# Kernel optimization log

Measured on AMD Instinct MI355X. Metric: run time of the kernel, lower is better.

Reference implementation:

```python
import jax, jax.numpy as jnp
import numpy as np

B, P, E, D = 256, 2048, 16, 2
HID, OUT = 128, 128
BN_EPS = 1e-5


def setup_inputs() -> dict:
    key = jax.random.key(0)
    ks = jax.random.split(key, 16)
    inp = {
        "barcode_h0": jax.random.normal(ks[0], (B, P, D), jnp.float32),
        "barcode_h0_count": jax.random.randint(ks[1], (B,), 0, P),
        "barcode_h1": jax.random.normal(ks[2], (B, P, D), jnp.float32),
        "barcode_h1_count": jax.random.randint(ks[3], (B,), 0, P),
        # SLayer params (one per homology dim): centers ~ U[0,1), log_sharpness = log(3.0)
        "centers0": jax.random.uniform(ks[4], (E, D), jnp.float32),
        "log_sharp0": jnp.full((E, D), np.log(3.0), jnp.float32),
        "centers1": jax.random.uniform(ks[5], (E, D), jnp.float32),
        "log_sharp1": jnp.full((E, D), np.log(3.0), jnp.float32),
        # head: Linear(2E -> HID, no bias), BN, ReLU, Linear(HID -> OUT, no bias), BN
        "W1": jax.random.normal(ks[6], (2 * E, HID), jnp.float32) / np.sqrt(2 * E),
        "gamma1": jnp.ones((HID,), jnp.float32),
        "beta1": jnp.zeros((HID,), jnp.float32),
        "W2": jax.random.normal(ks[7], (HID, OUT), jnp.float32) / np.sqrt(HID),
        "gamma2": jnp.ones((OUT,), jnp.float32),
        "beta2": jnp.zeros((OUT,), jnp.float32),
    }
    return inp


def _slayer(pts, counts, centers, log_sharp):
    # pts: [B,P,2], counts: [B], centers/log_sharp: [E,2]
    sharp = jax.nn.softplus(log_sharp) + 1e-6                       # [E,2]
    diff = pts[:, :, None, :] - centers[None, None, :, :]           # [B,P,E,2]
    resp = jnp.exp(-jnp.sum(sharp * diff * diff, axis=-1))          # [B,P,E]
    mask = (jnp.arange(pts.shape[1])[None, :] < counts[:, None]).astype(resp.dtype)
    return jnp.sum(resp * mask[:, :, None], axis=1)                 # [B,E]


def _batchnorm_train(x, gamma, beta):
    m = jnp.mean(x, axis=0)
    v = jnp.var(x, axis=0)  # biased, as torch uses for normalization
    return (x - m) * jax.lax.rsqrt(v + BN_EPS) * gamma + beta


def reference(barcode_h0, barcode_h0_count, barcode_h1, barcode_h1_count,
              centers0, log_sharp0, centers1, log_sharp1,
              W1, gamma1, beta1, W2, gamma2, beta2):
    f0 = _slayer(barcode_h0, barcode_h0_count, centers0, log_sharp0)  # [B,E]
    f1 = _slayer(barcode_h1, barcode_h1_count, centers1, log_sharp1)  # [B,E]
    x = jnp.concatenate([f0, f1], axis=1)                             # [B,2E]
    h = jax.nn.relu(_batchnorm_train(x @ W1, gamma1, beta1))          # [B,HID]
    y = _batchnorm_train(h @ W2, gamma2, beta2)                       # [B,OUT]
    norm = jnp.maximum(jnp.linalg.norm(y, axis=1, keepdims=True), 1e-12)
    return y / norm
```

## Files before the change

### kernel.cpp

```cpp
#include <hip/hip_runtime.h>

#define Bsz 256
#define Pn  2048
#define En  16
#define HIDn 128
#define OUTn 128
#define BN_EPS 1e-5f
#define NREP 16
#define POISON_I ((int)0xAAAAAAAA)


__device__ __forceinline__ void bar_sync(int* ctr) {
    __syncthreads();
    if (threadIdx.x == 0) {
        atomicCAS(ctr, POISON_I, 0);
        __hip_atomic_fetch_add(ctr, 1, __ATOMIC_RELEASE, __HIP_MEMORY_SCOPE_AGENT);
        while (__hip_atomic_load(ctr, __ATOMIC_RELAXED, __HIP_MEMORY_SCOPE_AGENT) < Bsz) {
            __builtin_amdgcn_s_sleep(1);
        }
    }
    __syncthreads();
}

__device__ __forceinline__ float coh_load(const float* p) {
    return __hip_atomic_load(p, __ATOMIC_RELAXED, __HIP_MEMORY_SCOPE_AGENT);
}

__global__ __launch_bounds__(256) void k_fused(
    const float* __restrict__ pts0, const int* __restrict__ cnt0,
    const float* __restrict__ pts1, const int* __restrict__ cnt1,
    const float* __restrict__ c0, const float* __restrict__ ls0,
    const float* __restrict__ c1, const float* __restrict__ ls1,
    const float* __restrict__ W1,
    const float* __restrict__ g1, const float* __restrict__ be1,
    const float* __restrict__ W2,
    const float* __restrict__ g2, const float* __restrict__ be2,
    float* __restrict__ stats,
    int* __restrict__ bars,
    float* __restrict__ out)
{
    __shared__ float4 cs[2][En];
    __shared__ float red[4][32];
    __shared__ float xrow[32];
    __shared__ float hrow[HIDn];
    __shared__ float part[4];

    const int tid = threadIdx.x;
    const int b   = blockIdx.x;

    float* sum1R   = stats;
    float* sumsq1R = stats + NREP * HIDn;
    float* sum2R   = stats + 2 * NREP * HIDn;
    float* sumsq2R = stats + 3 * NREP * HIDn;
    const int rep = (b & (NREP - 1)) * HIDn;

    if (tid < 32) {
        int h = tid >> 4, e = tid & 15;
        const float* C = h ? c1 : c0;
        const float* L = h ? ls1 : ls0;
        float zx = L[2 * e], zy = L[2 * e + 1];
        float sx = (zx > 20.f) ? zx : logf(1.f + expf(zx));
        float sy = (zy > 20.f) ? zy : logf(1.f + expf(zy));
        cs[h][e] = make_float4(C[2 * e], C[2 * e + 1], sx + 1e-6f, sy + 1e-6f);
    }
    __syncthreads();

    const int n0 = cnt0[b];
    const int n1 = cnt1[b];
    const float4* q0 = (const float4*)(pts0 + (size_t)b * Pn * 2);
    const float4* q1 = (const float4*)(pts1 + (size_t)b * Pn * 2);

    float4 f0[4], f1[4];
    #pragma unroll
    for (int i = 0; i < 4; i++) {
        f0[i] = q0[tid + (i << 8)];
        f1[i] = q1[tid + (i << 8)];
    }

    float g1v = 0.f, b1v = 0.f, g2v = 0.f, b2v = 0.f;
    if (tid < HIDn) { g1v = g1[tid]; b1v = be1[tid]; g2v = g2[tid]; b2v = be2[tid]; }

    float m0a[4], m0b[4], m1a[4], m1b[4];
    #pragma unroll
    for (int i = 0; i < 4; i++) {
        int p = (tid + (i << 8)) << 1;
        m0a[i] = (p     < n0) ? 1.f : 0.f;
        m0b[i] = (p + 1 < n0) ? 1.f : 0.f;
        m1a[i] = (p     < n1) ? 1.f : 0.f;
        m1b[i] = (p + 1 < n1) ? 1.f : 0.f;
    }

    float acc0[En], acc1[En];
    #pragma unroll
    for (int e = 0; e < En; e++) { acc0[e] = 0.f; acc1[e] = 0.f; }

    #pragma unroll
    for (int e = 0; e < En; e++) {
        float4 c = cs[0][e];
        float4 d = cs[1][e];
        float a0 = acc0[e], a1 = acc1[e];
        #pragma unroll
        for (int i = 0; i < 4; i++) {
            float dx, dy;
            dx = f0[i].x - c.x; dy = f0[i].y - c.y;
            a0 = fmaf(m0a[i], __expf(-(c.z * dx * dx + c.w * dy * dy)), a0);
            dx = f0[i].z - c.x; dy = f0[i].w - c.y;
            a0 = fmaf(m0b[i], __expf(-(c.z * dx * dx + c.w * dy * dy)), a0);
            dx = f1[i].x - d.x; dy = f1[i].y - d.y;
            a1 = fmaf(m1a[i], __expf(-(d.z * dx * dx + d.w * dy * dy)), a1);
            dx = f1[i].z - d.x; dy = f1[i].w - d.y;
            a1 = fmaf(m1b[i], __expf(-(d.z * dx * dx + d.w * dy * dy)), a1);
        }
        acc0[e] = a0; acc1[e] = a1;
    }

    #pragma unroll
    for (int e = 0; e < En; e++) {
        #pragma unroll
        for (int off = 32; off > 0; off >>= 1) {
            acc0[e] += __shfl_down(acc0[e], off, 64);
            acc1[e] += __shfl_down(acc1[e], off, 64);
        }
    }
    const int wave = tid >> 6, lane = tid & 63;
    if (lane == 0) {
        #pragma unroll
        for (int e = 0; e < En; e++) { red[wave][e] = acc0[e]; red[wave][16 + e] = acc1[e]; }
    }
    __syncthreads();
    if (tid < 32) xrow[tid] = red[0][tid] + red[1][tid] + red[2][tid] + red[3][tid];
    __syncthreads();

    float uv = 0.f;
    if (tid < HIDn) {
        #pragma unroll
        for (int k = 0; k < 32; k++) uv = fmaf(xrow[k], W1[k * HIDn + tid], uv);
        atomicAdd(&sum1R[rep + tid], uv);
        atomicAdd(&sumsq1R[rep + tid], uv * uv);
    }

    bar_sync(&bars[0]);

    if (tid < HIDn) {
        float s = 0.f, ss = 0.f;
        #pragma unroll
        for (int r = 0; r < NREP; r++) {
            s  += coh_load(&sum1R[r * HIDn + tid]);
            ss += coh_load(&sumsq1R[r * HIDn + tid]);
        }
        float m    = s * (1.f / Bsz);
        float var  = ss * (1.f / Bsz) - m * m;
        float rstd = rsqrtf(var + BN_EPS);
        hrow[tid]  = fmaxf((uv - m) * rstd * g1v + b1v, 0.f);
    }
    __syncthreads();

    float a = 0.f;
    if (tid < OUTn) {
        #pragma unroll 16
        for (int k = 0; k < HIDn; k++) a = fmaf(hrow[k], W2[k * OUTn + tid], a);
        atomicAdd(&sum2R[rep + tid], a);
        atomicAdd(&sumsq2R[rep + tid], a * a);
    }

    bar_sync(&bars[1]);

    float y = 0.f;
    if (tid < OUTn) {
        float s = 0.f, ss = 0.f;
        #pragma unroll
        for (int r = 0; r < NREP; r++) {
            s  += coh_load(&sum2R[r * HIDn + tid]);
            ss += coh_load(&sumsq2R[r * HIDn + tid]);
        }
        float m    = s * (1.f / Bsz);
        float var  = ss * (1.f / Bsz) - m * m;
        float rstd = rsqrtf(var + BN_EPS);
        y = (a - m) * rstd * g2v + b2v;
    }
    float sq = y * y;
    #pragma unroll
    for (int off = 32; off > 0; off >>= 1) sq += __shfl_down(sq, off, 64);
    if (lane == 0) part[wave] = sq;
    __syncthreads();
    if (tid < OUTn) {
        float total = part[0] + part[1] + part[2] + part[3];
        float norm  = fmaxf(sqrtf(total), 1e-12f);
        out[b * OUTn + tid] = y / norm;
    }
}

extern "C" void kernel_launch(void* const* d_in, const int* in_sizes, int n_in,
                              void* d_out, int out_size, void* d_ws, size_t ws_size,
                              hipStream_t stream) {
    const float* pts0 = (const float*)d_in[0];
    const int*   cnt0 = (const int*)  d_in[1];
    const float* pts1 = (const float*)d_in[2];
    const int*   cnt1 = (const int*)  d_in[3];
    const float* c0   = (const float*)d_in[4];
    const float* ls0  = (const float*)d_in[5];
    const float* c1   = (const float*)d_in[6];
    const float* ls1  = (const float*)d_in[7];
    const float* W1   = (const float*)d_in[8];
    const float* g1   = (const float*)d_in[9];
    const float* be1  = (const float*)d_in[10];
    const float* W2   = (const float*)d_in[11];
    const float* g2   = (const float*)d_in[12];
    const float* be2  = (const float*)d_in[13];
    float* out = (float*)d_out;

    float* stats = (float*)d_ws;
    int*   bars  = (int*)((float*)d_ws + 4 * NREP * HIDn);


    k_fused<<<Bsz, 256, 0, stream>>>(pts0, cnt0, pts1, cnt1,
                                     c0, ls0, c1, ls1,
                                     W1, g1, be1, W2, g2, be2,
                                     stats, bars, out);
}
```

Measured before the change: 110.4 us.

## Replace flat grid barrier with tree barrier and single-block BN stats broadcast

Replaces the flat 256-block atomic counter barrier with a two-level tree: blocks first arrive on one of 16 leaf counters, and the last arrival at the root computes the BatchNorm scale and shift once, then publishes them as packed 64-bit values and signals a finish flag. All other blocks spin on that single flag and read two floats instead of reducing 16 replicas each. W2 is prefetched into registers early and staged into 64KB of LDS to hide its global load latency. This relies on poisoned-workspace initial values and adds a large LDS footprint, which could limit co-residency of blocks.

```diff
diff --git a/kernel.cpp b/kernel.cpp
--- a/kernel.cpp
+++ b/kernel.cpp
@@ -7,22 +7,20 @@
 #define OUTn 128
 #define BN_EPS 1e-5f
 #define NREP 16
-#define POISON_I ((int)0xAAAAAAAA)
-
-
-__device__ __forceinline__ void bar_sync(int* ctr) {
-    __syncthreads();
-    if (threadIdx.x == 0) {
-        atomicCAS(ctr, POISON_I, 0);
-        __hip_atomic_fetch_add(ctr, 1, __ATOMIC_RELEASE, __HIP_MEMORY_SCOPE_AGENT);
-        while (__hip_atomic_load(ctr, __ATOMIC_RELAXED, __HIP_MEMORY_SCOPE_AGENT) < Bsz) {
-            __builtin_amdgcn_s_sleep(1);
-        }
-    }
-    __syncthreads();
-}
+#define NGRP 16
+#define POISON_U 0xAAAAAAAAu
+
+typedef unsigned int u32;
+typedef unsigned long long u64;
+
 
 __device__ __forceinline__ float coh_load(const float* p) {
+    return __hip_atomic_load(p, __ATOMIC_RELAXED, __HIP_MEMORY_SCOPE_AGENT);
+}
+__device__ __forceinline__ void coh_store64(u64* p, u64 v) {
+    __hip_atomic_store(p, v, __ATOMIC_RELAXED, __HIP_MEMORY_SCOPE_AGENT);
+}
+__device__ __forceinline__ u64 coh_load64(const u64* p) {
     return __hip_atomic_load(p, __ATOMIC_RELAXED, __HIP_MEMORY_SCOPE_AGENT);
 }
 
@@ -36,14 +34,17 @@
     const float* __restrict__ W2,
     const float* __restrict__ g2, const float* __restrict__ be2,
     float* __restrict__ stats,
-    int* __restrict__ bars,
+    u32* __restrict__ bars,
+    u64* __restrict__ mstd,
     float* __restrict__ out)
 {
+    __shared__ float W2ld[HIDn * OUTn];
     __shared__ float4 cs[2][En];
     __shared__ float red[4][32];
     __shared__ float xrow[32];
     __shared__ float hrow[HIDn];
     __shared__ float part[4];
+    __shared__ int   amFin;
 
     const int tid = threadIdx.x;
     const int b   = blockIdx.x;
@@ -53,6 +54,15 @@
     float* sum2R   = stats + 2 * NREP * HIDn;
     float* sumsq2R = stats + 3 * NREP * HIDn;
     const int rep = (b & (NREP - 1)) * HIDn;
+
+    u32* leaf0 = bars + (b >> 4) * 64;
+    u32* root0 = bars + 1024;
+    u32* fin0  = bars + 1088;
+    u32* leaf1 = bars + 2048 + (b >> 4) * 64;
+    u32* root1 = bars + 3072;
+    u32* fin1  = bars + 3136;
+    u64* mstd1 = mstd;
+    u64* mstd2 = mstd + HIDn;
 
     if (tid < 32) {
         int h = tid >> 4, e = tid & 15;
@@ -76,6 +86,10 @@
         f0[i] = q0[tid + (i << 8)];
         f1[i] = q1[tid + (i << 8)];
     }
+    const float4* W2v = (const float4*)W2;
+    float4 w2r[16];
+    #pragma unroll
+    for (int i = 0; i < 16; i++) w2r[i] = W2v[tid + (i << 8)];
 
     float g1v = 0.f, b1v = 0.f, g2v = 0.f, b2v = 0.f;
     if (tid < HIDn) { g1v = g1[tid]; b1v = be1[tid]; g2v = g2[tid]; b2v = be2[tid]; }
@@ -115,6 +129,10 @@
     }
 
     #pragma unroll
+    for (int i = 0; i < 16; i++)
+        ((float4*)W2ld)[tid + (i << 8)] = w2r[i];
+
+    #pragma unroll
     for (int e = 0; e < En; e++) {
         #pragma unroll
         for (int off = 32; off > 0; off >>= 1) {
@@ -139,44 +157,98 @@
         atomicAdd(&sumsq1R[rep + tid], uv * uv);
     }
 
-    bar_sync(&bars[0]);
+    __syncthreads();
+    if (tid == 0) {
+        u32 lo = __hip_atomic_fetch_add(leaf0, 1u, __ATOMIC_ACQ_REL, __HIP_MEMORY_SCOPE_AGENT);
+        int f = 0;
+        if (lo == POISON_U + (Bsz / NGRP - 1)) {
+            u32 ro = __hip_atomic_fetch_add(root0, 1u, __ATOMIC_ACQ_REL, __HIP_MEMORY_SCOPE_AGENT);
+            f = (ro == POISON_U + (NGRP - 1));
+        }
+        amFin = f;
+    }
+    __syncthreads();
+    if (amFin) {
+        if (tid < HIDn) {
+            float s = 0.f, ss = 0.f;
+            #pragma unroll
+            for (int r = 0; r < NREP; r++) s  += coh_load(&sum1R[r * HIDn + tid]);
+            #pragma unroll
+            for (int r = 0; r < NREP; r++) ss += coh_load(&sumsq1R[r * HIDn + tid]);
+            float m    = s * (1.f / Bsz);
+            float var  = ss * (1.f / Bsz) - m * m;
+            float A    = rsqrtf(var + BN_EPS) * g1v;
+            float Bc   = b1v - m * A;
+            coh_store64(&mstd1[tid], (u64)__float_as_uint(A) |
+                                     ((u64)__float_as_uint(Bc) << 32));
+        }
+        __syncthreads();
+        if (tid == 0)
+            __hip_atomic_fetch_add(fin0, 1u, __ATOMIC_RELEASE, __HIP_MEMORY_SCOPE_AGENT);
+    }
+    if (tid == 0) {
+        while (__hip_atomic_load(fin0, __ATOMIC_RELAXED, __HIP_MEMORY_SCOPE_AGENT)
+               != POISON_U + 1u) __builtin_amdgcn_s_sleep(1);
+    }
+    __syncthreads();
 
     if (tid < HIDn) {
-        float s = 0.f, ss = 0.f;
-        #pragma unroll
-        for (int r = 0; r < NREP; r++) {
-            s  += coh_load(&sum1R[r * HIDn + tid]);
-            ss += coh_load(&sumsq1R[r * HIDn + tid]);
-        }
-        float m    = s * (1.f / Bsz);
-        float var  = ss * (1.f / Bsz) - m * m;
-        float rstd = rsqrtf(var + BN_EPS);
-        hrow[tid]  = fmaxf((uv - m) * rstd * g1v + b1v, 0.f);
+        u64 pk = coh_load64(&mstd1[tid]);
+        float A  = __uint_as_float((u32)pk);
+        float Bc = __uint_as_float((u32)(pk >> 32));
+        hrow[tid] = fmaxf(fmaf(uv, A, Bc), 0.f);
     }
     __syncthreads();
 
     float a = 0.f;
     if (tid < OUTn) {
         #pragma unroll 16
-        for (int k = 0; k < HIDn; k++) a = fmaf(hrow[k], W2[k * OUTn + tid], a);
+        for (int k = 0; k < HIDn; k++) a = fmaf(hrow[k], W2ld[k * OUTn + tid], a);
         atomicAdd(&sum2R[rep + tid], a);
         atomicAdd(&sumsq2R[rep + tid], a * a);
     }
 
-    bar_sync(&bars[1]);
+    __syncthreads();
+    if (tid == 0) {
+        u32 lo = __hip_atomic_fetch_add(leaf1, 1u, __ATOMIC_ACQ_REL, __HIP_MEMORY_SCOPE_AGENT);
+        int f = 0;
+        if (lo == POISON_U + (Bsz / NGRP - 1)) {
+            u32 ro = __hip_atomic_fetch_add(root1, 1u, __ATOMIC_ACQ_REL, __HIP_MEMORY_SCOPE_AGENT);
+            f = (ro == POISON_U + (NGRP - 1));
+        }
+        amFin = f;
+    }
+    __syncthreads();
+    if (amFin) {
+        if (tid < HIDn) {
+            float s = 0.f, ss = 0.f;
+            #pragma unroll
+            for (int r = 0; r < NREP; r++) s  += coh_load(&sum2R[r * HIDn + tid]);
+            #pragma unroll
+            for (int r = 0; r < NREP; r++) ss += coh_load(&sumsq2R[r * HIDn + tid]);
+            float m    = s * (1.f / Bsz);
+            float var  = ss * (1.f / Bsz) - m * m;
+            float A    = rsqrtf(var + BN_EPS) * g2v;
+            float Bc   = b2v - m * A;
+            coh_store64(&mstd2[tid], (u64)__float_as_uint(A) |
+                                     ((u64)__float_as_uint(Bc) << 32));
+        }
+        __syncthreads();
+        if (tid == 0)
+            __hip_atomic_fetch_add(fin1, 1u, __ATOMIC_RELEASE, __HIP_MEMORY_SCOPE_AGENT);
+    }
+    if (tid == 0) {
+        while (__hip_atomic_load(fin1, __ATOMIC_RELAXED, __HIP_MEMORY_SCOPE_AGENT)
+               != POISON_U + 1u) __builtin_amdgcn_s_sleep(1);
+    }
+    __syncthreads();
 
     float y = 0.f;
     if (tid < OUTn) {
-        float s = 0.f, ss = 0.f;
-        #pragma unroll
-        for (int r = 0; r < NREP; r++) {
-            s  += coh_load(&sum2R[r * HIDn + tid]);
-            ss += coh_load(&sumsq2R[r * HIDn + tid]);
-        }
-        float m    = s * (1.f / Bsz);
-        float var  = ss * (1.f / Bsz) - m * m;
-        float rstd = rsqrtf(var + BN_EPS);
-        y = (a - m) * rstd * g2v + b2v;
+        u64 pk = coh_load64(&mstd2[tid]);
+        float A  = __uint_as_float((u32)pk);
+        float Bc = __uint_as_float((u32)(pk >> 32));
+        y = fmaf(a, A, Bc);
     }
     float sq = y * y;
     #pragma unroll
@@ -210,11 +282,12 @@
     float* out = (float*)d_out;
 
     float* stats = (float*)d_ws;
-    int*   bars  = (int*)((float*)d_ws + 4 * NREP * HIDn);
+    u32*   bars  = (u32*)((float*)d_ws + 4 * NREP * HIDn);
+    u64*   mstd  = (u64*)(bars + 4096);
 
 
     k_fused<<<Bsz, 256, 0, stream>>>(pts0, cnt0, pts1, cnt1,
                                      c0, ls0, c1, ls1,
                                      W1, g1, be1, W2, g2, be2,
-                                     stats, bars, out);
-}
+                                     stats, bars, mstd, out);
+}
```

Measured after the change: 105.7 us. -4.3%, faster.
